# Performance work log

Measured on AMD Instinct MI355X. Metric: run time of the kernel, lower is better.

## Reference

```python
import jax, jax.numpy as jnp
import numpy as np

B, HH, WW = 8, 56, 56
N = HH * WW            # 3136 tokens
DIM, NH, SR = 512, 8, 7
HDIM = DIM // 2        # 256
LDIM = DIM - HDIM      # 256
DH = LDIM // NH        # 32
SCALE = DIM ** -0.5
EPS = 1e-5


def _dwconv(x, w):
    # depthwise 3x3, stride 1, SAME (= padding k//2): x [B,C,H,W], w [C,1,3,3]
    return jax.lax.conv_general_dilated(x, w, (1, 1), 'SAME',
                                        feature_group_count=x.shape[1],
                                        dimension_numbers=('NCHW', 'OIHW', 'NCHW'))


def _bn(x, g, b, m, v):
    # inference BatchNorm2d
    s = g * jax.lax.rsqrt(v + EPS)
    return (x - m[None, :, None, None]) * s[None, :, None, None] + b[None, :, None, None]


def _avg_pool(x, k):
    return jax.lax.reduce_window(x, 0.0, jax.lax.add, (1, 1, k, k), (1, 1, k, k), 'VALID') / (k * k)


def _max_pool(x, k):
    return jax.lax.reduce_window(x, -jnp.inf, jax.lax.max, (1, 1, k, k), (1, 1, k, k), 'VALID')


def setup_inputs() -> dict:
    key = jax.random.key(0)
    ks = jax.random.split(key, 32)
    d = {}
    d['x'] = jax.random.normal(ks[0], (B, N, DIM), jnp.float32)
    d['proj_v_w'] = jax.random.normal(ks[1], (LDIM, HDIM), jnp.float32) / np.sqrt(HDIM).astype(np.float32)
    d['conv1_w'] = jax.random.normal(ks[2], (LDIM, 1, 3, 3), jnp.float32) / 3.0
    d['conv2_w'] = jax.random.normal(ks[3], (LDIM, 1, 3, 3), jnp.float32) / 3.0
    d['conv3_w'] = jax.random.normal(ks[4], (HDIM, LDIM, 1, 1), jnp.float32) / np.sqrt(LDIM).astype(np.float32)
    d['conv3_b'] = jax.random.normal(ks[5], (HDIM,), jnp.float32) * 0.1
    d['v_conv_w'] = jax.random.normal(ks[6], (LDIM, 1, 3, 3), jnp.float32) / 3.0
    d['proj_w'] = jax.random.normal(ks[7], (DIM, DIM), jnp.float32) / np.sqrt(DIM).astype(np.float32)
    d['proj_b'] = jax.random.normal(ks[8], (DIM,), jnp.float32) * 0.1
    i = 9
    for pre, c in (('bn1', LDIM), ('bn2', LDIM), ('bn3', HDIM), ('vbn', LDIM)):
        d[pre + '_g'] = jax.random.uniform(ks[i], (c,), jnp.float32, 0.8, 1.2)
        d[pre + '_b'] = jax.random.normal(ks[i + 1], (c,), jnp.float32) * 0.1
        d[pre + '_m'] = jax.random.normal(ks[i + 2], (c,), jnp.float32) * 0.1
        d[pre + '_v'] = jax.random.uniform(ks[i + 3], (c,), jnp.float32, 0.5, 1.5)
        i += 4
    return d


def reference(x, proj_v_w, conv1_w, conv2_w, conv3_w, conv3_b, v_conv_w, proj_w, proj_b,
              bn1_g, bn1_b, bn1_m, bn1_v, bn2_g, bn2_b, bn2_m, bn2_v,
              bn3_g, bn3_b, bn3_m, bn3_v, vbn_g, vbn_b, vbn_m, vbn_v):
    x_high_in = x[..., :HDIM]                       # [B,N,HDIM]
    v = x_high_in @ proj_v_w.T                      # [B,N,LDIM]
    xh = v.reshape(B, HH, WW, LDIM).transpose(0, 3, 1, 2)   # [B,LDIM,H,W]
    xh = _bn(_dwconv(xh, conv1_w), bn1_g, bn1_b, bn1_m, bn1_v)
    q1 = _avg_pool(xh, SR)                          # [B,LDIM,8,8]
    q2 = _max_pool(xh, SR)
    xh = jax.nn.gelu(xh, approximate=False)
    xh = _bn(_dwconv(xh, conv2_w), bn2_g, bn2_b, bn2_m, bn2_v)
    k1 = _avg_pool(xh, SR)
    k2 = _max_pool(xh, SR)
    xh = jax.lax.conv_general_dilated(xh, conv3_w, (1, 1), 'SAME',
                                      dimension_numbers=('NCHW', 'OIHW', 'NCHW')) + conv3_b[None, :, None, None]
    xh = _bn(xh, bn3_g, bn3_b, bn3_m, bn3_v)
    xh = jax.nn.gelu(xh, approximate=False)
    x_high = xh.reshape(B, HDIM, N).transpose(0, 2, 1)      # [B,N,HDIM]

    hq, wq = HH // SR, WW // SR
    nq = hq * wq                                    # 64 pooled tokens

    def heads(t):                                   # [B,LDIM,hq,wq] -> [B,NH,nq,DH]
        return t.reshape(B, NH, DH, nq).transpose(0, 1, 3, 2)

    q = jnp.concatenate([heads(q1), heads(q2)], axis=-1)    # [B,NH,nq,2*DH]
    k = jnp.concatenate([heads(k1), heads(k2)], axis=-1)
    vh = v.reshape(B, N, NH, DH).transpose(0, 2, 1, 3)      # [B,NH,N,DH]

    attn = jnp.einsum('bhqd,bhkd->bhqk', q, k)              # [B,NH,nq,nq]
    attn = attn.reshape(B * NH, nq, hq, wq)
    attn = jax.image.resize(attn, (B * NH, nq, HH, WW), method='bilinear', antialias=False) * SCALE
    attn = attn.reshape(B, NH, nq, N)
    attn = jax.nn.softmax(attn, axis=-1)

    out = jnp.einsum('bhqn,bhnd->bhqd', attn, vh)           # [B,NH,nq,DH]
    out = out.reshape(B, NH, hq, wq, DH).transpose(0, 1, 4, 2, 3).reshape(B, LDIM, hq, wq)
    out = jax.image.resize(out, (B, LDIM, HH, WW), method='bilinear', antialias=False)
    out = _bn(_dwconv(out, v_conv_w), vbn_g, vbn_b, vbn_m, vbn_v)
    x_low = out.reshape(B, LDIM, N).transpose(0, 2, 1)      # [B,N,LDIM]

    y = jnp.concatenate([x_high, x_low], axis=-1) @ proj_w.T + proj_b
    return y
```

## Files before the change

kernel.cpp:

```cpp
#include <hip/hip_runtime.h>
#include <math.h>

#define BB 8
#define HH 56
#define WWD 56
#define NN 3136
#define CC 256
#define DIMM 512
#define NHEAD 8
#define NQ 64
#define EPSF 1e-5f
#define SCALEF 0.04419417382415922f

typedef __attribute__((ext_vector_type(8))) short short8;
typedef __attribute__((ext_vector_type(4))) short short4v;
typedef __attribute__((ext_vector_type(4))) float floatx4;

__device__ __forceinline__ float gelu_f(float x) {
    float z = x * 0.70710678118654752f;
    float a = fabsf(z);
    float t = __builtin_amdgcn_rcpf(1.f + 0.3275911f * a);
    float p = t * (0.254829592f + t * (-0.284496736f + t * (1.421413741f +
              t * (-1.453152027f + t * 1.061405429f))));
    float e = exp2f(-1.44269504f * a * a);
    float erfa = 1.f - p * e;
    float erfz = copysignf(erfa, z);
    return 0.5f * x * (1.f + erfz);
}
__device__ __forceinline__ unsigned short f2bf(float f) {
    union { float f; unsigned u; } v; v.f = f;
    return (unsigned short)((v.u + 0x7fffu + ((v.u >> 16) & 1u)) >> 16);
}
__device__ __forceinline__ float bf2f(unsigned short u) {
    union { unsigned u; float f; } v; v.u = ((unsigned)u) << 16;
    return v.f;
}

__device__ __forceinline__ void stage_w_f32(const float* __restrict__ wsrc,
                                            int rowlen, int c0, int k0,
                                            short* __restrict__ Bs, int tid) {
    int c = tid >> 1;
    int ob = (tid & 1) * 4;
    const float* src = wsrc + (size_t)(c0 + c) * rowlen + k0 + ob * 8;
    short* dst = &Bs[c * 72 + ob * 8];
#pragma unroll
    for (int i2 = 0; i2 < 4; i2++) {
        floatx4 f0 = *(const floatx4*)(src + i2 * 8);
        floatx4 f1 = *(const floatx4*)(src + i2 * 8 + 4);
        short8 pk;
        pk[0] = (short)f2bf(f0[0]); pk[1] = (short)f2bf(f0[1]);
        pk[2] = (short)f2bf(f0[2]); pk[3] = (short)f2bf(f0[3]);
        pk[4] = (short)f2bf(f1[0]); pk[5] = (short)f2bf(f1[1]);
        pk[6] = (short)f2bf(f1[2]); pk[7] = (short)f2bf(f1[3]);
        *(short8*)(dst + i2 * 8) = pk;
    }
}

__global__ __launch_bounds__(256) void gemm_v_mfma(
    const float* __restrict__ x, const float* __restrict__ wsrc,
    unsigned short* __restrict__ v16) {
    __shared__ short Ws[128 * 72];
    __shared__ short Xs[128 * 72];
    int n0 = blockIdx.y * 128, c0 = blockIdx.x * 128;
    int tid = threadIdx.x;
    int lane = tid & 63, wv = tid >> 6;
    int wc = wv >> 1, wn = wv & 1;
    int quad = lane >> 4, l16 = lane & 15;
    floatx4 zero = {0.f, 0.f, 0.f, 0.f};
    floatx4 acc[4][4];
#pragma unroll
    for (int ci = 0; ci < 4; ci++)
#pragma unroll
        for (int ni = 0; ni < 4; ni++) acc[ci][ni] = zero;

    for (int k0 = 0; k0 < 256; k0 += 64) {
        {
            int m = tid >> 1;
            int ob = (tid & 1) * 4;
            const float* src = x + (size_t)(n0 + m) * DIMM + k0 + ob * 8;
            short* dst = &Xs[m * 72 + ob * 8];
#pragma unroll
            for (int i2 = 0; i2 < 4; i2++) {
                floatx4 f0 = *(const floatx4*)(src + i2 * 8);
                floatx4 f1 = *(const floatx4*)(src + i2 * 8 + 4);
                short8 pk;
                pk[0] = (short)f2bf(f0[0]); pk[1] = (short)f2bf(f0[1]);
                pk[2] = (short)f2bf(f0[2]); pk[3] = (short)f2bf(f0[3]);
                pk[4] = (short)f2bf(f1[0]); pk[5] = (short)f2bf(f1[1]);
                pk[6] = (short)f2bf(f1[2]); pk[7] = (short)f2bf(f1[3]);
                *(short8*)(dst + i2 * 8) = pk;
            }
        }
        stage_w_f32(wsrc, 256, c0, k0, Ws, tid);
        __syncthreads();
#pragma unroll
        for (int kc = 0; kc < 2; kc++) {
            short8 af[4], bf[4];
#pragma unroll
            for (int ci = 0; ci < 4; ci++)
                af[ci] = *(const short8*)&Ws[(wc * 64 + ci * 16 + l16) * 72 + (kc * 4 + quad) * 8];
#pragma unroll
            for (int ni = 0; ni < 4; ni++)
                bf[ni] = *(const short8*)&Xs[(wn * 64 + ni * 16 + l16) * 72 + (kc * 4 + quad) * 8];
#pragma unroll
            for (int ci = 0; ci < 4; ci++)
#pragma unroll
                for (int ni = 0; ni < 4; ni++)
                    acc[ci][ni] = __builtin_amdgcn_mfma_f32_16x16x32_bf16(
                        af[ci], bf[ni], acc[ci][ni], 0, 0, 0);
        }
        __syncthreads();
    }
#pragma unroll
    for (int ni = 0; ni < 4; ni++) {
        int ng = n0 + wn * 64 + ni * 16 + l16;
        int b = ng / NN, n = ng - b * NN;
#pragma unroll
        for (int ci = 0; ci < 4; ci++) {
#pragma unroll
            for (int r = 0; r < 4; r++) {
                int c = c0 + wc * 64 + ci * 16 + quad * 4 + r;
                v16[((size_t)b * CC + c) * NN + n] = f2bf(acc[ci][ni][r]);
            }
        }
    }
}

__device__ __forceinline__ float dw3x3g(const float* __restrict__ Us, int lr,
                                        int x, bool ym, bool yp,
                                        float w0, float w1, float w2, float w3,
                                        float w4, float w5, float w6, float w7,
                                        float w8) {
    bool xm = x > 0, xp = x < 55;
    const float* r1 = &Us[(lr - 1) * 57 + x];
    const float* r2 = &Us[lr * 57 + x];
    const float* r3 = &Us[(lr + 1) * 57 + x];
    float acc = r2[0] * w4;
    if (xm) acc += r2[-1] * w3;
    if (xp) acc += r2[1] * w5;
    if (ym) {
        acc += r1[0] * w1;
        if (xm) acc += r1[-1] * w0;
        if (xp) acc += r1[1] * w2;
    }
    if (yp) {
        acc += r3[0] * w7;
        if (xm) acc += r3[-1] * w6;
        if (xp) acc += r3[1] * w8;
    }
    return acc;
}

__global__ __launch_bounds__(256) void dwconv2x_k(
    const unsigned short* __restrict__ in,
    const float* __restrict__ w1c, const float* __restrict__ g1,
    const float* __restrict__ b1, const float* __restrict__ m1,
    const float* __restrict__ v1,
    const float* __restrict__ w2c, const float* __restrict__ g2,
    const float* __restrict__ b2, const float* __restrict__ m2,
    const float* __restrict__ v2,
    unsigned short* __restrict__ out,
    float* __restrict__ oavg1, float* __restrict__ omax1,
    float* __restrict__ oavg2, float* __restrict__ omax2) {
    __shared__ float Us[18 * 57];
    __shared__ float Cs[16 * 57];
    int bid = blockIdx.x;
    int bc = bid >> 2, chunk = bid & 3;
    int c = bc & 255;
    int r0 = chunk * 14;
    int tid = threadIdx.x;
    const unsigned short* ip = in + (size_t)bc * NN;

    int gl0 = max(r0 - 2, 0), gh0 = min(r0 + 15, 55);
    int nin = (gh0 - gl0 + 1) * 56;
    const unsigned short* ipb = ip + gl0 * 56;
    {
        int e = tid * 4;
        if (e < nin) {
            short4v pk = *(const short4v*)(const short*)(ipb + e);
#pragma unroll
            for (int j = 0; j < 4; j++) {
                int el = e + j;
                int ry = el / 56, x = el - ry * 56;
                int lr = (gl0 + ry) - (r0 - 2);
                Us[lr * 57 + x] = bf2f((unsigned short)pk[j]);
            }
        }
    }
    float w0 = w1c[c * 9 + 0], w1 = w1c[c * 9 + 1], w2 = w1c[c * 9 + 2];
    float w3 = w1c[c * 9 + 3], w4 = w1c[c * 9 + 4], w5 = w1c[c * 9 + 5];
    float w6 = w1c[c * 9 + 6], w7 = w1c[c * 9 + 7], w8 = w1c[c * 9 + 8];
    float s = g1[c] * rsqrtf(v1[c] + EPSF);
    float sh = b1[c] - m1[c] * s;
    __syncthreads();
    int c1lo = max(r0 - 1, 0), c1hi = min(r0 + 14, 55);
    int n1 = (c1hi - c1lo + 1) * 56;
    for (int i = tid; i < n1; i += 256) {
        int ry = i / 56, x = i - ry * 56;
        int gr = c1lo + ry;
        int liu = gr - (r0 - 2);
        float acc = dw3x3g(Us, liu, x, gr > 0, gr < 55,
                           w0, w1, w2, w3, w4, w5, w6, w7, w8);
        Cs[(gr - (r0 - 1)) * 57 + x] = acc * s + sh;
    }
    __syncthreads();
    if (tid < 16) {
        int qy = 2 * chunk + (tid >> 3), qx = tid & 7;
        const float* p0 = &Cs[(qy * 7 - (r0 - 1)) * 57 + qx * 7];
        float sm = 0.f, mx = -INFINITY;
#pragma unroll
        for (int py = 0; py < 7; py++)
#pragma unroll
            for (int px = 0; px < 7; px++) {
                float t = p0[py * 57 + px];
                sm += t;
                mx = fmaxf(mx, t);
            }
        oavg1[(size_t)bc * 64 + qy * 8 + qx] = sm * (1.f / 49.f);
        omax1[(size_t)bc * 64 + qy * 8 + qx] = mx;
    }
    for (int i = tid; i < n1; i += 256) {
        int ry = i / 56, x = i - ry * 56;
        int lr1 = (c1lo + ry) - (r0 - 1);
        Us[lr1 * 57 + x] = gelu_f(Cs[lr1 * 57 + x]);
    }
    w0 = w2c[c * 9 + 0]; w1 = w2c[c * 9 + 1]; w2 = w2c[c * 9 + 2];
    w3 = w2c[c * 9 + 3]; w4 = w2c[c * 9 + 4]; w5 = w2c[c * 9 + 5];
    w6 = w2c[c * 9 + 6]; w7 = w2c[c * 9 + 7]; w8 = w2c[c * 9 + 8];
    s = g2[c] * rsqrtf(v2[c] + EPSF);
    sh = b2[c] - m2[c] * s;
    __syncthreads();
    unsigned short* op = out + (size_t)bc * NN;
    for (int i = tid; i < 14 * 56; i += 256) {
        int ry = i / 56, x = i - ry * 56;
        int gr = r0 + ry;
        int lg = ry + 1;
        float val = dw3x3g(Us, lg, x, gr > 0, gr < 55,
                           w0, w1, w2, w3, w4, w5, w6, w7, w8) * s + sh;
        Cs[ry * 57 + x] = val;
        op[gr * 56 + x] = f2bf(val);
    }
    __syncthreads();
    if (tid < 16) {
        int qy = 2 * chunk + (tid >> 3), qx = tid & 7;
        const float* p0 = &Cs[((qy * 7) - r0) * 57 + qx * 7];
        float sm = 0.f, mx = -INFINITY;
#pragma unroll
        for (int py = 0; py < 7; py++)
#pragma unroll
            for (int px = 0; px < 7; px++) {
                float t = p0[py * 57 + px];
                sm += t;
                mx = fmaxf(mx, t);
            }
        oavg2[(size_t)bc * 64 + qy * 8 + qx] = sm * (1.f / 49.f);
        omax2[(size_t)bc * 64 + qy * 8 + qx] = mx;
    }
}

__global__ __launch_bounds__(256) void conv3_mfma(
    const unsigned short* __restrict__ xin, const float* __restrict__ wsrc,
    const float* __restrict__ bias, const float* __restrict__ g,
    const float* __restrict__ bparm, const float* __restrict__ mm,
    const float* __restrict__ vvv, unsigned short* __restrict__ out16) {
    __shared__ short As[128 * 72];
    __shared__ short Bs[128 * 72];
    int m0 = blockIdx.y * 128, c0 = blockIdx.x * 128;
    int tid = threadIdx.x;
    int lane = tid & 63, wv = tid >> 6;
    int wm = wv >> 1, wc = wv & 1;
    int quad = lane >> 4, l16 = lane & 15;
    floatx4 zero = {0.f, 0.f, 0.f, 0.f};
    floatx4 acc[4][4];
#pragma unroll
    for (int mi = 0; mi < 4; mi++)
#pragma unroll
        for (int ci = 0; ci < 4; ci++) acc[mi][ci] = zero;

    for (int k0 = 0; k0 < 256; k0 += 64) {
#pragma unroll
        for (int i2 = 0; i2 < 4; i2++) {
            int mo = i2 * 4 + wv;
            int kk = lane;
            int m8 = m0 + mo * 8;
            int b8 = m8 / NN, n8 = m8 - b8 * NN;
            short8 pk = *(const short8*)(const short*)(
                xin + ((size_t)b8 * CC + (k0 + kk)) * NN + n8);
            short* dst = &As[(mo * 8) * 72 + kk];
#pragma unroll
            for (int j = 0; j < 8; j++) dst[j * 72] = pk[j];
        }
        stage_w_f32(wsrc, CC, c0, k0, Bs, tid);
        __syncthreads();
#pragma unroll
        for (int kc = 0; kc < 2; kc++) {
            short8 af[4], bf[4];
#pragma unroll
            for (int mi = 0; mi < 4; mi++)
                af[mi] = *(const short8*)&As[(wm * 64 + mi * 16 + l16) * 72 + (kc * 4 + quad) * 8];
#pragma unroll
            for (int ci = 0; ci < 4; ci++)
                bf[ci] = *(const short8*)&Bs[(wc * 64 + ci * 16 + l16) * 72 + (kc * 4 + quad) * 8];
#pragma unroll
            for (int mi = 0; mi < 4; mi++)
#pragma unroll
                for (int ci = 0; ci < 4; ci++)
                    acc[mi][ci] = __builtin_amdgcn_mfma_f32_16x16x32_bf16(
                        af[mi], bf[ci], acc[mi][ci], 0, 0, 0);
        }
        __syncthreads();
    }
#pragma unroll
    for (int ci = 0; ci < 4; ci++) {
        int co = c0 + wc * 64 + ci * 16 + l16;
        float s = g[co] * rsqrtf(vvv[co] + EPSF);
        float sh = bparm[co] - mm[co] * s;
        float bi = bias[co];
#pragma unroll
        for (int mi = 0; mi < 4; mi++) {
            int mbase = m0 + wm * 64 + mi * 16 + quad * 4;
#pragma unroll
            for (int r = 0; r < 4; r++) {
                float val = gelu_f((acc[mi][ci][r] + bi) * s + sh);
                out16[(size_t)(mbase + r) * CC + co] = f2bf(val);
            }
        }
    }
}

__global__ __launch_bounds__(256) void attn_qk_k(
    const float* __restrict__ q1, const float* __restrict__ q2,
    const float* __restrict__ k1, const float* __restrict__ k2,
    float* __restrict__ attn_s, float* __restrict__ mq) {
    int b = blockIdx.x >> 3, h = blockIdx.x & 7;
    __shared__ float Qs[64][64];
    __shared__ float Ks[64][64];
    __shared__ float pm[4][64];
    int tid = threadIdx.x;
#pragma unroll
    for (int l = 0; l < 16; l++) {
        int e = tid + 256 * l;
        int dt = e >> 6, i = e & 63;
        int d = dt & 31;
        const float* sq = (dt < 32) ? q1 : q2;
        const float* sk = (dt < 32) ? k1 : k2;
        Qs[dt][i] = sq[((size_t)b * CC + h * 32 + d) * NQ + i];
        Ks[dt][i] = sk[((size_t)b * CC + h * 32 + d) * NQ + i];
    }
    __syncthreads();
    int i = tid & 63, jg = tid >> 6;
    float acc[16] = {};
    for (int dt = 0; dt < 64; dt++) {
        float qv = Qs[dt][i];
#pragma unroll
        for (int t = 0; t < 16; t++) acc[t] += qv * Ks[dt][jg * 16 + t];
    }
    float mx = -INFINITY;
#pragma unroll
    for (int t = 0; t < 16; t++) {
        acc[t] *= SCALEF;
        mx = fmaxf(mx, acc[t]);
    }
    pm[jg][i] = mx;
    float* outp = attn_s + (((size_t)(b * 8 + h) * 64 + i) * 64) + jg * 16;
#pragma unroll
    for (int t = 0; t < 16; t++) outp[t] = acc[t];
    __syncthreads();
    if (tid < 64) {
        float m = fmaxf(fmaxf(pm[0][tid], pm[1][tid]),
                        fmaxf(pm[2][tid], pm[3][tid]));
        mq[(size_t)(b * 8 + h) * 64 + tid] = m;
    }
}

__global__ __launch_bounds__(256) void attn_pv_k(
    const float* __restrict__ attn_s, const float* __restrict__ mq,
    const unsigned short* __restrict__ v16,
    float* __restrict__ part_O, float* __restrict__ part_rs) {
    __shared__ float asub[64][68];
    __shared__ unsigned short Vs[32][456];
    __shared__ short po4[448][4];
    __shared__ float pw4[448][4];
    int s = blockIdx.x, bh = blockIdx.y;
    int b = bh >> 3, h = bh & 7;
    int tid = threadIdx.x;
    int lane = tid & 63, wv = tid >> 6;
    int quad = lane >> 4, l16 = lane & 15;
    int q = wv * 16 + l16;
    float Mv = mq[(size_t)bh * 64 + q];
    {
        int qq = tid & 63, jg = tid >> 6;
        const float* src = attn_s + ((size_t)bh * 64 + qq) * 64 + jg * 16;
        float* dst = &asub[qq][jg * 16];
#pragma unroll
        for (int t = 0; t < 4; t++)
            *(floatx4*)(dst + t * 4) = *(const floatx4*)(src + t * 4);
    }
    {
        int d = tid >> 3, o0 = tid & 7;
        const unsigned short* vp =
            v16 + ((size_t)(b * CC + h * 32 + d)) * NN + s * 448;
#pragma unroll
        for (int t = 0; t < 7; t++) {
            int oc = o0 + t * 8;
            *(short8*)&Vs[d][oc * 8] = *(const short8*)(const short*)(vp + oc * 8);
        }
    }
    for (int idx = tid; idx < 448; idx += 256) {
        int n = s * 448 + idx;
        int oy = n / WWD, ox = n - oy * WWD;
        float sy = (oy + 0.5f) * 0.14285714285714285f - 0.5f;
        float sx = (ox + 0.5f) * 0.14285714285714285f - 0.5f;
        float fy0 = floorf(sy), fx0 = floorf(sx);
        int y0 = (int)fy0, x0 = (int)fx0;
        float fy = sy - fy0, fx = sx - fx0;
        int y0c = max(y0, 0), y1c = min(y0 + 1, 7);
        int x0c = max(x0, 0), x1c = min(x0 + 1, 7);
        po4[idx][0] = (short)(y0c * 8 + x0c);
        po4[idx][1] = (short)(y0c * 8 + x1c);
        po4[idx][2] = (short)(y1c * 8 + x0c);
        po4[idx][3] = (short)(y1c * 8 + x1c);
        pw4[idx][0] = (1.f - fy) * (1.f - fx);
        pw4[idx][1] = (1.f - fy) * fx;
        pw4[idx][2] = fy * (1.f - fx);
        pw4[idx][3] = fy * fx;
    }
    __syncthreads();
    floatx4 zero = {0.f, 0.f, 0.f, 0.f};
    floatx4 acc0 = zero, acc1 = zero;
    float rsum = 0.f;
    for (int cch = 0; cch < 7; cch++) {
#pragma unroll
        for (int kc = 0; kc < 2; kc++) {
            int col = cch * 64 + kc * 32 + quad * 8;
            short8 af;
#pragma unroll
            for (int j = 0; j < 8; j++) {
                int np = col + j;
                float val = pw4[np][0] * asub[q][po4[np][0]]
                          + pw4[np][1] * asub[q][po4[np][1]]
                          + pw4[np][2] * asub[q][po4[np][2]]
                          + pw4[np][3] * asub[q][po4[np][3]];
                float p = exp2f((val - Mv) * 1.44269504f);
                rsum += p;
                af[j] = (short)f2bf(p);
            }
            short8 bf0 = *(const short8*)&Vs[l16][col];
            short8 bf1 = *(const short8*)&Vs[16 + l16][col];
            acc0 = __builtin_amdgcn_mfma_f32_16x16x32_bf16(af, bf0, acc0, 0, 0, 0);
            acc1 = __builtin_amdgcn_mfma_f32_16x16x32_bf16(af, bf1, acc1, 0, 0, 0);
        }
    }
    rsum += __shfl_xor(rsum, 16, 64);
    rsum += __shfl_xor(rsum, 32, 64);
    size_t base = ((size_t)bh * 7 + s) * 64;
    if (lane < 16) part_rs[base + wv * 16 + lane] = rsum;
#pragma unroll
    for (int nt = 0; nt < 2; nt++) {
        floatx4 a = nt ? acc1 : acc0;
#pragma unroll
        for (int r = 0; r < 4; r++) {
            int qo = wv * 16 + quad * 4 + r;
            part_O[(base + qo) * 32 + nt * 16 + l16] = a[r];
        }
    }
}

__global__ __launch_bounds__(256) void upconv_k(
    const float* __restrict__ part_O, const float* __restrict__ part_rs,
    const float* __restrict__ w,
    const float* __restrict__ g, const float* __restrict__ bparm,
    const float* __restrict__ m, const float* __restrict__ v,
    unsigned short* __restrict__ xlow16) {
    __shared__ float ts[64];
    __shared__ float Us[16 * 57];
    int bid = blockIdx.x;
    int bc = bid >> 2, chunk = bid & 3;
    int c = bc & 255;
    int r0 = chunk * 14;
    int tid = threadIdx.x;
    if (tid < 64) {
        int h = c >> 5, d = c & 31;
        int bh = (bc >> 8) * 8 + h;
        float o = 0.f, rs = 0.f;
        for (int s7 = 0; s7 < 7; s7++) {
            size_t base = ((size_t)bh * 7 + s7) * 64 + tid;
            o += part_O[base * 32 + d];
            rs += part_rs[base];
        }
        ts[tid] = o / rs;
    }
    __syncthreads();
    int blo = max(r0 - 1, 0), bhi = min(r0 + 14, 55);
    int nb = (bhi - blo + 1) * 56;
    for (int i = tid; i < nb; i += 256) {
        int ry = i / 56, x = i - ry * 56;
        int gr = blo + ry;
        float sy = (gr + 0.5f) * 0.14285714285714285f - 0.5f;
        float sx = (x + 0.5f) * 0.14285714285714285f - 0.5f;
        float fy0 = floorf(sy), fx0 = floorf(sx);
        int y0 = (int)fy0, x0 = (int)fx0;
        float fy = sy - fy0, fx = sx - fx0;
        int y0c = max(y0, 0), y1c = min(y0 + 1, 7);
        int x0c = max(x0, 0), x1c = min(x0 + 1, 7);
        float v00 = ts[y0c * 8 + x0c], v01 = ts[y0c * 8 + x1c];
        float v10 = ts[y1c * 8 + x0c], v11 = ts[y1c * 8 + x1c];
        Us[(gr - (r0 - 1)) * 57 + x] =
            (1.f - fy) * ((1.f - fx) * v00 + fx * v01) +
            fy * ((1.f - fx) * v10 + fx * v11);
    }
    float w0 = w[c * 9 + 0], w1 = w[c * 9 + 1], w2 = w[c * 9 + 2];
    float w3 = w[c * 9 + 3], w4 = w[c * 9 + 4], w5 = w[c * 9 + 5];
    float w6 = w[c * 9 + 6], w7 = w[c * 9 + 7], w8 = w[c * 9 + 8];
    float s = g[c] * rsqrtf(v[c] + EPSF);
    float sh = bparm[c] - m[c] * s;
    __syncthreads();
    unsigned short* op = xlow16 + (size_t)bc * NN;
    for (int i = tid; i < 14 * 56; i += 256) {
        int ry = i / 56, x = i - ry * 56;
        int gr = r0 + ry;
        float val = dw3x3g(Us, ry + 1, x, gr > 0, gr < 55,
                           w0, w1, w2, w3, w4, w5, w6, w7, w8);
        op[gr * 56 + x] = f2bf(val * s + sh);
    }
}

__global__ __launch_bounds__(256) void proj_mfma(
    const unsigned short* __restrict__ xh16, const unsigned short* __restrict__ xl16,
    const float* __restrict__ wsrc, const float* __restrict__ bias,
    float* __restrict__ y) {
    __shared__ short As[128 * 72];
    __shared__ short Bs[128 * 72];
    int m0 = blockIdx.y * 128, c0 = blockIdx.x * 128;
    int tid = threadIdx.x;
    int lane = tid & 63, wv = tid >> 6;
    int wm = wv >> 1, wc = wv & 1;
    int quad = lane >> 4, l16 = lane & 15;
    floatx4 zero = {0.f, 0.f, 0.f, 0.f};
    floatx4 acc[4][4];
#pragma unroll
    for (int mi = 0; mi < 4; mi++)
#pragma unroll
        for (int ci = 0; ci < 4; ci++) acc[mi][ci] = zero;

    for (int k0 = 0; k0 < 512; k0 += 64) {
        if (k0 < 256) {
#pragma unroll
            for (int i2 = 0; i2 < 4; i2++) {
                int idx = tid + 256 * i2;
                int m = idx >> 3, o = idx & 7;
                *(short8*)&As[m * 72 + o * 8] =
                    *(const short8*)(const short*)(xh16 + (size_t)(m0 + m) * CC + k0 + o * 8);
            }
        } else {
#pragma unroll
            for (int i2 = 0; i2 < 4; i2++) {
                int mo = i2 * 4 + wv;
                int kk = lane;
                int m8 = m0 + mo * 8;
                int b8 = m8 / NN, n8 = m8 - b8 * NN;
                short8 pk = *(const short8*)(const short*)(
                    xl16 + ((size_t)b8 * CC + (k0 - 256 + kk)) * NN + n8);
                short* dst = &As[(mo * 8) * 72 + kk];
#pragma unroll
                for (int j = 0; j < 8; j++) dst[j * 72] = pk[j];
            }
        }
        stage_w_f32(wsrc, DIMM, c0, k0, Bs, tid);
        __syncthreads();
#pragma unroll
        for (int kc = 0; kc < 2; kc++) {
            short8 af[4], bf[4];
#pragma unroll
            for (int mi = 0; mi < 4; mi++)
                af[mi] = *(const short8*)&As[(wm * 64 + mi * 16 + l16) * 72 + (kc * 4 + quad) * 8];
#pragma unroll
            for (int ci = 0; ci < 4; ci++)
                bf[ci] = *(const short8*)&Bs[(wc * 64 + ci * 16 + l16) * 72 + (kc * 4 + quad) * 8];
#pragma unroll
            for (int mi = 0; mi < 4; mi++)
#pragma unroll
                for (int ci = 0; ci < 4; ci++)
                    acc[mi][ci] = __builtin_amdgcn_mfma_f32_16x16x32_bf16(
                        af[mi], bf[ci], acc[mi][ci], 0, 0, 0);
        }
        __syncthreads();
    }
#pragma unroll
    for (int mi = 0; mi < 4; mi++) {
        int mbase = m0 + wm * 64 + mi * 16 + quad * 4;
#pragma unroll
        for (int ci = 0; ci < 4; ci++) {
            int co = c0 + wc * 64 + ci * 16 + l16;
            float bi = bias[co];
#pragma unroll
            for (int r = 0; r < 4; r++)
                y[(size_t)(mbase + r) * DIMM + co] = acc[mi][ci][r] + bi;
        }
    }
}

extern "C" void kernel_launch(void* const* d_in, const int* in_sizes, int n_in,
                              void* d_out, int out_size, void* d_ws, size_t ws_size,
                              hipStream_t stream) {
    const float* x        = (const float*)d_in[0];
    const float* proj_v_w = (const float*)d_in[1];
    const float* conv1_w  = (const float*)d_in[2];
    const float* conv2_w  = (const float*)d_in[3];
    const float* conv3_w  = (const float*)d_in[4];
    const float* conv3_b  = (const float*)d_in[5];
    const float* v_conv_w = (const float*)d_in[6];
    const float* proj_w   = (const float*)d_in[7];
    const float* proj_b   = (const float*)d_in[8];
    const float* bn1_g = (const float*)d_in[9],  *bn1_b = (const float*)d_in[10];
    const float* bn1_m = (const float*)d_in[11], *bn1_v = (const float*)d_in[12];
    const float* bn2_g = (const float*)d_in[13], *bn2_b = (const float*)d_in[14];
    const float* bn2_m = (const float*)d_in[15], *bn2_v = (const float*)d_in[16];
    const float* bn3_g = (const float*)d_in[17], *bn3_b = (const float*)d_in[18];
    const float* bn3_m = (const float*)d_in[19], *bn3_v = (const float*)d_in[20];
    const float* vbn_g = (const float*)d_in[21], *vbn_b = (const float*)d_in[22];
    const float* vbn_m = (const float*)d_in[23], *vbn_v = (const float*)d_in[24];

    const size_t big = (size_t)BB * CC * NN;
    unsigned short* v16    = (unsigned short*)d_ws;
    unsigned short* bufA16 = v16 + big;
    unsigned short* bufB16 = bufA16 + big;
    unsigned short* xh16   = bufB16 + big;
    unsigned short* xlow16 = xh16 + big;
    float* small = (float*)(xlow16 + big);
    float* q1 = small;
    float* q2 = q1 + (size_t)BB * CC * NQ;
    float* k1 = q2 + (size_t)BB * CC * NQ;
    float* k2 = k1 + (size_t)BB * CC * NQ;
    float* attn_s = k2 + (size_t)BB * CC * NQ;
    float* out_s  = attn_s + (size_t)BB * NHEAD * NQ * NQ;
    float* part_O = out_s + (size_t)BB * CC * NQ;
    float* part_rs = part_O + (size_t)64 * 7 * 64 * 32;
    float* mq = part_rs + (size_t)64 * 7 * 64;

    gemm_v_mfma<<<dim3(2, 196), 256, 0, stream>>>(x, proj_v_w, v16);
    dwconv2x_k<<<BB * CC * 4, 256, 0, stream>>>(
        v16, conv1_w, bn1_g, bn1_b, bn1_m, bn1_v,
        conv2_w, bn2_g, bn2_b, bn2_m, bn2_v, bufB16, q1, q2, k1, k2);
    conv3_mfma<<<dim3(2, 196), 256, 0, stream>>>(bufB16, conv3_w, conv3_b,
                                                 bn3_g, bn3_b, bn3_m, bn3_v, xh16);
    attn_qk_k<<<64, 256, 0, stream>>>(q1, q2, k1, k2, attn_s, mq);
    attn_pv_k<<<dim3(7, 64), 256, 0, stream>>>(attn_s, mq, v16, part_O, part_rs);
    upconv_k<<<BB * CC * 4, 256, 0, stream>>>(part_O, part_rs, v_conv_w,
                                              vbn_g, vbn_b, vbn_m, vbn_v, xlow16);
    proj_mfma<<<dim3(4, 196), 256, 0, stream>>>(xh16, xlow16, proj_w, proj_b,
                                                (float*)d_out);
}
```

Before: 303.4 us.

## Co-schedule conv3 GEMM with attention kernels and pre-cast weights to bf16

Splits the conv3 GEMM tiles across the small attention QK and PV launches as extra blocks, so those low-occupancy kernels share the GPU with independent GEMM work. The first launch gains extra blocks that convert proj_w and conv3_w to bf16 once, and the conv3 and proj GEMMs then stage the bf16 weights directly instead of converting fp32 in every tile. proj grid order is swapped so consecutive blocks walk m for a fixed c. This costs extra workspace, larger shared-memory footprints for the merged kernels, and possible load imbalance between the heterogeneous block types.

```diff
diff --git a/kernel.cpp b/kernel.cpp
--- a/kernel.cpp
+++ b/kernel.cpp
@@ -56,13 +56,26 @@
     }
 }
 
-__global__ __launch_bounds__(256) void gemm_v_mfma(
-    const float* __restrict__ x, const float* __restrict__ wsrc,
-    unsigned short* __restrict__ v16) {
+__global__ __launch_bounds__(256) void l1_gemmv_cast(
+    const float* __restrict__ x, const float* __restrict__ wv_f32,
+    unsigned short* __restrict__ v16,
+    const float* __restrict__ proj_w, const float* __restrict__ conv3_w,
+    unsigned short* __restrict__ w16p, unsigned short* __restrict__ w16c3) {
     __shared__ short Ws[128 * 72];
     __shared__ short Xs[128 * 72];
-    int n0 = blockIdx.y * 128, c0 = blockIdx.x * 128;
+    int bid = blockIdx.x;
     int tid = threadIdx.x;
+    if (bid >= 392) {
+        int start = (bid - 392) * 1024;
+        int end = start + 1024;
+        if (end > 327680) end = 327680;
+        for (int i = start + tid; i < end; i += 256) {
+            if (i < 262144) w16p[i] = f2bf(proj_w[i]);
+            else w16c3[i - 262144] = f2bf(conv3_w[i - 262144]);
+        }
+        return;
+    }
+    int n0 = (bid % 196) * 128, c0 = (bid / 196) * 128;
     int lane = tid & 63, wv = tid >> 6;
     int wc = wv >> 1, wn = wv & 1;
     int quad = lane >> 4, l16 = lane & 15;
@@ -91,7 +104,7 @@
                 *(short8*)(dst + i2 * 8) = pk;
             }
         }
-        stage_w_f32(wsrc, 256, c0, k0, Ws, tid);
+        stage_w_f32(wv_f32, 256, c0, k0, Ws, tid);
         __syncthreads();
 #pragma unroll
         for (int kc = 0; kc < 2; kc++) {
@@ -258,14 +271,15 @@
     }
 }
 
-__global__ __launch_bounds__(256) void conv3_mfma(
-    const unsigned short* __restrict__ xin, const float* __restrict__ wsrc,
+__device__ void conv3_body(
+    char* smem, int mct,
+    const unsigned short* __restrict__ xin, const unsigned short* __restrict__ w16,
     const float* __restrict__ bias, const float* __restrict__ g,
     const float* __restrict__ bparm, const float* __restrict__ mm,
     const float* __restrict__ vvv, unsigned short* __restrict__ out16) {
-    __shared__ short As[128 * 72];
-    __shared__ short Bs[128 * 72];
-    int m0 = blockIdx.y * 128, c0 = blockIdx.x * 128;
+    short* As = (short*)smem;
+    short* Bs = (short*)(smem + 18432);
+    int m0 = (mct % 196) * 128, c0 = (mct / 196) * 128;
     int tid = threadIdx.x;
     int lane = tid & 63, wv = tid >> 6;
     int wm = wv >> 1, wc = wv & 1;
@@ -290,7 +304,13 @@
 #pragma unroll
             for (int j = 0; j < 8; j++) dst[j * 72] = pk[j];
         }
-        stage_w_f32(wsrc, CC, c0, k0, Bs, tid);
+#pragma unroll
+        for (int i2 = 0; i2 < 4; i2++) {
+            int idx = tid + 256 * i2;
+            int c = idx >> 3, o = idx & 7;
+            *(short8*)&Bs[c * 72 + o * 8] =
+                *(const short8*)(const short*)(w16 + (size_t)(c0 + c) * CC + k0 + o * 8);
+        }
         __syncthreads();
 #pragma unroll
         for (int kc = 0; kc < 2; kc++) {
@@ -328,15 +348,25 @@
     }
 }
 
-__global__ __launch_bounds__(256) void attn_qk_k(
+__global__ __launch_bounds__(256) void l3_qk_conv3(
     const float* __restrict__ q1, const float* __restrict__ q2,
     const float* __restrict__ k1, const float* __restrict__ k2,
-    float* __restrict__ attn_s, float* __restrict__ mq) {
-    int b = blockIdx.x >> 3, h = blockIdx.x & 7;
-    __shared__ float Qs[64][64];
-    __shared__ float Ks[64][64];
-    __shared__ float pm[4][64];
+    float* __restrict__ attn_s, float* __restrict__ mq,
+    const unsigned short* __restrict__ xin, const unsigned short* __restrict__ w16,
+    const float* __restrict__ bias, const float* __restrict__ g,
+    const float* __restrict__ bparm, const float* __restrict__ mm,
+    const float* __restrict__ vvv, unsigned short* __restrict__ out16) {
+    __shared__ __align__(16) char smem[36864];
+    int bid = blockIdx.x;
     int tid = threadIdx.x;
+    if (bid >= 64) {
+        conv3_body(smem, bid - 64, xin, w16, bias, g, bparm, mm, vvv, out16);
+        return;
+    }
+    float (*Qs)[64] = (float(*)[64])smem;
+    float (*Ks)[64] = (float(*)[64])(smem + 16384);
+    float (*pm)[64] = (float(*)[64])(smem + 32768);
+    int b = bid >> 3, h = bid & 7;
 #pragma unroll
     for (int l = 0; l < 16; l++) {
         int e = tid + 256 * l;
@@ -373,17 +403,27 @@
     }
 }
 
-__global__ __launch_bounds__(256) void attn_pv_k(
+__global__ __launch_bounds__(256) void l4_pv_conv3(
     const float* __restrict__ attn_s, const float* __restrict__ mq,
     const unsigned short* __restrict__ v16,
-    float* __restrict__ part_O, float* __restrict__ part_rs) {
-    __shared__ float asub[64][68];
-    __shared__ unsigned short Vs[32][456];
-    __shared__ short po4[448][4];
-    __shared__ float pw4[448][4];
-    int s = blockIdx.x, bh = blockIdx.y;
+    float* __restrict__ part_O, float* __restrict__ part_rs,
+    const unsigned short* __restrict__ xin, const unsigned short* __restrict__ w16,
+    const float* __restrict__ bias, const float* __restrict__ g,
+    const float* __restrict__ bparm, const float* __restrict__ mm,
+    const float* __restrict__ vvv, unsigned short* __restrict__ out16) {
+    __shared__ __align__(16) char smem[57344];
+    int bid = blockIdx.x;
+    int tid = threadIdx.x;
+    if (bid >= 448) {
+        conv3_body(smem, 128 + bid - 448, xin, w16, bias, g, bparm, mm, vvv, out16);
+        return;
+    }
+    float (*asub)[68] = (float(*)[68])smem;
+    unsigned short (*Vs)[456] = (unsigned short(*)[456])(smem + 17408);
+    short (*po4)[4] = (short(*)[4])(smem + 46592);
+    float (*pw4)[4] = (float(*)[4])(smem + 50176);
+    int s = bid % 7, bh = bid / 7;
     int b = bh >> 3, h = bh & 7;
-    int tid = threadIdx.x;
     int lane = tid & 63, wv = tid >> 6;
     int quad = lane >> 4, l16 = lane & 15;
     int q = wv * 16 + l16;
@@ -527,11 +567,11 @@
 
 __global__ __launch_bounds__(256) void proj_mfma(
     const unsigned short* __restrict__ xh16, const unsigned short* __restrict__ xl16,
-    const float* __restrict__ wsrc, const float* __restrict__ bias,
+    const unsigned short* __restrict__ w16, const float* __restrict__ bias,
     float* __restrict__ y) {
     __shared__ short As[128 * 72];
     __shared__ short Bs[128 * 72];
-    int m0 = blockIdx.y * 128, c0 = blockIdx.x * 128;
+    int m0 = blockIdx.x * 128, c0 = blockIdx.y * 128;
     int tid = threadIdx.x;
     int lane = tid & 63, wv = tid >> 6;
     int wm = wv >> 1, wc = wv & 1;
@@ -566,7 +606,13 @@
                 for (int j = 0; j < 8; j++) dst[j * 72] = pk[j];
             }
         }
-        stage_w_f32(wsrc, DIMM, c0, k0, Bs, tid);
+#pragma unroll
+        for (int i2 = 0; i2 < 4; i2++) {
+            int idx = tid + 256 * i2;
+            int c = idx >> 3, o = idx & 7;
+            *(short8*)&Bs[c * 72 + o * 8] =
+                *(const short8*)(const short*)(w16 + (size_t)(c0 + c) * DIMM + k0 + o * 8);
+        }
         __syncthreads();
 #pragma unroll
         for (int kc = 0; kc < 2; kc++) {
@@ -637,17 +683,22 @@
     float* part_O = out_s + (size_t)BB * CC * NQ;
     float* part_rs = part_O + (size_t)64 * 7 * 64 * 32;
     float* mq = part_rs + (size_t)64 * 7 * 64;
-
-    gemm_v_mfma<<<dim3(2, 196), 256, 0, stream>>>(x, proj_v_w, v16);
+    unsigned short* w16c3 = (unsigned short*)(mq + 64 * 64);
+    unsigned short* w16p  = w16c3 + 65536;
+
+    l1_gemmv_cast<<<712, 256, 0, stream>>>(x, proj_v_w, v16,
+                                           proj_w, conv3_w, w16p, w16c3);
     dwconv2x_k<<<BB * CC * 4, 256, 0, stream>>>(
         v16, conv1_w, bn1_g, bn1_b, bn1_m, bn1_v,
         conv2_w, bn2_g, bn2_b, bn2_m, bn2_v, bufB16, q1, q2, k1, k2);
-    conv3_mfma<<<dim3(2, 196), 256, 0, stream>>>(bufB16, conv3_w, conv3_b,
-                                                 bn3_g, bn3_b, bn3_m, bn3_v, xh16);
-    attn_qk_k<<<64, 256, 0, stream>>>(q1, q2, k1, k2, attn_s, mq);
-    attn_pv_k<<<dim3(7, 64), 256, 0, stream>>>(attn_s, mq, v16, part_O, part_rs);
+    l3_qk_conv3<<<64 + 128, 256, 0, stream>>>(
+        q1, q2, k1, k2, attn_s, mq,
+        bufB16, w16c3, conv3_b, bn3_g, bn3_b, bn3_m, bn3_v, xh16);
+    l4_pv_conv3<<<448 + 264, 256, 0, stream>>>(
+        attn_s, mq, v16, part_O, part_rs,
+        bufB16, w16c3, conv3_b, bn3_g, bn3_b, bn3_m, bn3_v, xh16);
     upconv_k<<<BB * CC * 4, 256, 0, stream>>>(part_O, part_rs, v_conv_w,
                                               vbn_g, vbn_b, vbn_m, vbn_v, xlow16);
-    proj_mfma<<<dim3(4, 196), 256, 0, stream>>>(xh16, xlow16, proj_w, proj_b,
+    proj_mfma<<<dim3(196, 4), 256, 0, stream>>>(xh16, xlow16, w16p, proj_b,
                                                 (float*)d_out);
 }
```

Result: faster. 288.5 us (-4.9%).
